# Optimization experiments

Hardware: AMD Instinct MI355X
Metric: run time of the kernel (lower is better)

The kernel has to match this reference:

```python
import jax, jax.numpy as jnp
import numpy as np

THRESHOLD = 0.4


def _pair_feat(xs, xd):
    # pair_mode='both': [src, dst, |src-dst|, src*dst] along feature axis
    return jnp.concatenate([xs, xd, jnp.abs(xs - xd), xs * xd], axis=-1)


def _mlp(pf, W1, b1, W2, b2):
    h = jax.nn.relu(pf @ W1 + b1)
    return (h @ W2 + b2)[..., 0]


def setup_inputs() -> dict:
    key = jax.random.key(0)
    k1, k2, k3, k4, k5 = jax.random.split(key, 5)
    N, F, E, H = 1024, 64, 65536, 32
    x = jax.random.normal(k1, (N, F), dtype=jnp.float32)
    edge_index = jax.random.randint(k2, (2, E), 0, N, dtype=jnp.int64)
    edge_index_global = jax.random.randint(k3, (2, E), 0, N, dtype=jnp.int64)
    W1 = jax.random.normal(k4, (4 * F, H), dtype=jnp.float32) * (1.0 / np.sqrt(4 * F))
    b1 = jnp.zeros((H,), dtype=jnp.float32)
    W2 = jax.random.normal(k5, (H, 1), dtype=jnp.float32) * (1.0 / np.sqrt(H))
    b2 = jnp.zeros((1,), dtype=jnp.float32)
    return {"x": x, "edge_index": edge_index, "edge_index_global": edge_index_global,
            "W1": W1, "b1": b1, "W2": W2, "b2": b2}


def reference(x, edge_index, edge_index_global, W1, b1, W2, b2):
    # ---- sparse edge branch ----
    xs = x[edge_index[0]]            # [E, F]
    xd = x[edge_index[1]]            # [E, F]
    pf = _pair_feat(xs, xd)          # [E, 4F]
    edge_logits = _mlp(pf, W1, b1, W2, b2)        # [E]
    edge_probs = jax.nn.sigmoid(edge_logits)      # [E]
    edge_actions = (edge_probs > THRESHOLD).astype(x.dtype)  # [E]
    # (new_edge_index / raw_edge_index in the original are data-dependent
    #  boolean selections of edge columns; the mask is edge_actions==1.)

    # ---- dense all-pairs branch (train=True) ----
    N, F = x.shape
    xi = jnp.broadcast_to(x[:, None, :], (N, N, F))  # src of pair (i,j)
    xj = jnp.broadcast_to(x[None, :, :], (N, N, F))  # dst of pair (i,j)
    pf_all = _pair_feat(xi, xj)                      # [N, N, 4F] -- dominant intermediate
    logits_all = _mlp(pf_all, W1, b1, W2, b2)        # [N, N]
    P = jax.nn.sigmoid(logits_all)                   # [N, N]

    return edge_probs, edge_actions, P
```

## Files before the change

kernel.cpp:

```cpp
#include <hip/hip_runtime.h>
#include <hip/hip_bf16.h>
#include <math.h>

#define NN 1024
#define FD 64
#define EE 65536
#define HD 32

typedef __attribute__((ext_vector_type(8))) short short8;
typedef __attribute__((ext_vector_type(4))) float floatx4;

__device__ __forceinline__ float sigmoid_f(float z) {
  return 1.0f / (1.0f + expf(-z));
}
__device__ __forceinline__ float sigmoid_fast(float z) {
  return 1.0f / (1.0f + __expf(-z));
}

__device__ __forceinline__ unsigned pack_bf16_trunc(float hi, float lo) {
  unsigned a = __builtin_bit_cast(unsigned, hi);
  unsigned b = __builtin_bit_cast(unsigned, lo);
  return __builtin_amdgcn_perm(a, b, 0x07060302u);
}

__device__ __forceinline__ short8 pack8(const float* v) {
  union { unsigned u[4]; short8 s; } p;
#pragma unroll
  for (int t = 0; t < 4; ++t) p.u[t] = pack_bf16_trunc(v[2 * t + 1], v[2 * t]);
  return p.s;
}

struct Frag3 { short8 a0, a1, a2; };

__device__ __forceinline__ Frag3 split_pack(const float* v) {
  float r[8], r2[8];
#pragma unroll
  for (int t = 0; t < 8; ++t) {
    const unsigned uv = __builtin_bit_cast(unsigned, v[t]);
    const float f0 = __builtin_bit_cast(float, uv & 0xFFFF0000u);
    const float rr = v[t] - f0;
    const unsigned ur = __builtin_bit_cast(unsigned, rr);
    const float f1 = __builtin_bit_cast(float, ur & 0xFFFF0000u);
    r[t] = rr;
    r2[t] = rr - f1;
  }
  Frag3 f;
  f.a0 = pack8(v);
  f.a1 = pack8(r);
  f.a2 = pack8(r2);
  return f;
}

__global__ __launch_bounds__(256) void pre_kernel3(
    const float* __restrict__ x, const float* __restrict__ W1,
    const float* __restrict__ b1, float* __restrict__ pre,
    short* __restrict__ Wt0, short* __restrict__ Wt1, short* __restrict__ Wt2) {
  const int blk = blockIdx.x;
  const int t = threadIdx.x;
  if (blk < 256) {
    const int node = blk * 4 + (t >> 6);
    const int which = (t >> 5) & 1;
    const int h = t & 31;
    const float* xr = x + node * FD;
    const float* wp = W1 + which * FD * HD + h;
    float a0 = which ? 0.0f : b1[h], a1 = 0.0f, a2 = 0.0f, a3 = 0.0f;
#pragma unroll
    for (int f = 0; f < FD; f += 4) {
      a0 = fmaf(xr[f + 0], wp[(f + 0) * HD], a0);
      a1 = fmaf(xr[f + 1], wp[(f + 1) * HD], a1);
      a2 = fmaf(xr[f + 2], wp[(f + 2) * HD], a2);
      a3 = fmaf(xr[f + 3], wp[(f + 3) * HD], a3);
    }
    pre[which * (NN * HD) + node * HD + h] = (a0 + a1) + (a2 + a3);
  } else {
    for (int idx = t; idx < 32 * 128; idx += 256) {
      const int h = idx >> 7;
      const int k = idx & 127;
      const int f = k & 63;
      const int b = 2 + (k >> 6);
      const float v = W1[(b * FD + f) * HD + h];
      const unsigned uv = __builtin_bit_cast(unsigned, v);
      const unsigned u0 = uv & 0xFFFF0000u;
      const float f0 = __builtin_bit_cast(float, u0);
      const float r = v - f0;
      const unsigned u1 = __builtin_bit_cast(unsigned, r) & 0xFFFF0000u;
      const float f1 = __builtin_bit_cast(float, u1);
      const float r2 = r - f1;
      const unsigned u2 = __builtin_bit_cast(unsigned, r2) & 0xFFFF0000u;
      Wt0[idx] = (short)(u0 >> 16);
      Wt1[idx] = (short)(u1 >> 16);
      Wt2[idx] = (short)(u2 >> 16);
    }
  }
}

__device__ __forceinline__ void edge_chunk(
    const float* feat, const short* __restrict__ Wt0,
    const short* __restrict__ Wt1, const short* __restrict__ Wt2,
    int c, int q, int kc, floatx4& acc0, floatx4& acc1) {
  const Frag3 B = split_pack(feat);
  const int off0 = c * 128 + kc * 32 + q * 8;
  const int off1 = (16 + c) * 128 + kc * 32 + q * 8;
  const short8 A00 = *(const short8*)(Wt0 + off0);
  const short8 A01 = *(const short8*)(Wt1 + off0);
  const short8 A02 = *(const short8*)(Wt2 + off0);
  const short8 A10 = *(const short8*)(Wt0 + off1);
  const short8 A11 = *(const short8*)(Wt1 + off1);
  const short8 A12 = *(const short8*)(Wt2 + off1);
  acc0 = __builtin_amdgcn_mfma_f32_16x16x32_bf16(A00, B.a0, acc0, 0, 0, 0);
  acc0 = __builtin_amdgcn_mfma_f32_16x16x32_bf16(A01, B.a0, acc0, 0, 0, 0);
  acc0 = __builtin_amdgcn_mfma_f32_16x16x32_bf16(A02, B.a0, acc0, 0, 0, 0);
  acc0 = __builtin_amdgcn_mfma_f32_16x16x32_bf16(A00, B.a1, acc0, 0, 0, 0);
  acc0 = __builtin_amdgcn_mfma_f32_16x16x32_bf16(A01, B.a1, acc0, 0, 0, 0);
  acc0 = __builtin_amdgcn_mfma_f32_16x16x32_bf16(A00, B.a2, acc0, 0, 0, 0);
  acc1 = __builtin_amdgcn_mfma_f32_16x16x32_bf16(A10, B.a0, acc1, 0, 0, 0);
  acc1 = __builtin_amdgcn_mfma_f32_16x16x32_bf16(A11, B.a0, acc1, 0, 0, 0);
  acc1 = __builtin_amdgcn_mfma_f32_16x16x32_bf16(A12, B.a0, acc1, 0, 0, 0);
  acc1 = __builtin_amdgcn_mfma_f32_16x16x32_bf16(A10, B.a1, acc1, 0, 0, 0);
  acc1 = __builtin_amdgcn_mfma_f32_16x16x32_bf16(A11, B.a1, acc1, 0, 0, 0);
  acc1 = __builtin_amdgcn_mfma_f32_16x16x32_bf16(A10, B.a2, acc1, 0, 0, 0);
}

#define DENSE_BLOCKS 520

__global__ __launch_bounds__(256, 3) void fused_mfma_kernel(
    const float* __restrict__ x, const int* __restrict__ eidx,
    const float* __restrict__ pre, const short* __restrict__ Wt0,
    const short* __restrict__ Wt1, const short* __restrict__ Wt2,
    const float* __restrict__ W2, const float* __restrict__ b2,
    float* __restrict__ out, float* __restrict__ outP) {
  __shared__ float mir[4][256];
  const int lane = threadIdx.x & 63;
  const int w = threadIdx.x >> 6;
  const int q = lane >> 4;
  const int c = lane & 15;

  if (blockIdx.x < DENSE_BLOCKS) {
    const int T = blockIdx.x * 4 + w;
    int a = (int)((sqrtf(8.0f * (float)T + 1.0f) - 1.0f) * 0.5f);
    while ((a + 1) * (a + 2) / 2 <= T) ++a;
    while (a * (a + 1) / 2 > T) --a;
    const int b = T - a * (a + 1) / 2;
    const int j0 = a * 16;
    const int i0 = b * 16;
    const bool offdiag = (a != b);

    short8 Af[2][4];
#pragma unroll
    for (int n = 0; n < 2; ++n)
#pragma unroll
      for (int s = 0; s < 4; ++s)
        Af[n][s] = *(const short8*)(Wt0 + (n * 16 + c) * 128 + s * 32 + q * 8);

    const float* xj = x + (size_t)(j0 + c) * FD;
    float jA[8], jB[8];
#pragma unroll
    for (int t = 0; t < 4; ++t) {
      jA[t] = xj[q * 8 + t];      jA[4 + t] = xj[q * 8 + 4 + t];
      jB[t] = xj[32 + q * 8 + t]; jB[4 + t] = xj[32 + q * 8 + 4 + t];
    }

    const floatx4 psA_j = *(const floatx4*)(pre + (j0 + c) * HD + q * 4);
    const floatx4 psB_j = *(const floatx4*)(pre + (j0 + c) * HD + 16 + q * 4);
    const floatx4 pdA_j = *(const floatx4*)(pre + NN * HD + (j0 + c) * HD + q * 4);
    const floatx4 pdB_j = *(const floatx4*)(pre + NN * HD + (j0 + c) * HD + 16 + q * 4);
    const floatx4 w2A = *(const floatx4*)(W2 + q * 4);
    const floatx4 w2B = *(const floatx4*)(W2 + 16 + q * 4);
    const float b2v = b2[0];

    for (int ii = 0; ii < 16; ++ii) {
      const int i = i0 + ii;
      const float* xi = x + (size_t)i * FD;
      const floatx4 psA_i = *(const floatx4*)(pre + i * HD + q * 4);
      const floatx4 psB_i = *(const floatx4*)(pre + i * HD + 16 + q * 4);
      floatx4 acc0 = {0.0f, 0.0f, 0.0f, 0.0f};
      floatx4 acc1 = {0.0f, 0.0f, 0.0f, 0.0f};

      {
        const floatx4 i0v = *(const floatx4*)(xi + q * 8);
        const floatx4 i1v = *(const floatx4*)(xi + q * 8 + 4);
        float ad[8], pr[8];
#pragma unroll
        for (int t = 0; t < 4; ++t) {
          ad[t] = fabsf(i0v[t] - jA[t]);         pr[t] = i0v[t] * jA[t];
          ad[4 + t] = fabsf(i1v[t] - jA[4 + t]); pr[4 + t] = i1v[t] * jA[4 + t];
        }
        const short8 fad = pack8(ad);
        const short8 fpr = pack8(pr);
        acc0 = __builtin_amdgcn_mfma_f32_16x16x32_bf16(Af[0][0], fad, acc0, 0, 0, 0);
        acc1 = __builtin_amdgcn_mfma_f32_16x16x32_bf16(Af[1][0], fad, acc1, 0, 0, 0);
        acc0 = __builtin_amdgcn_mfma_f32_16x16x32_bf16(Af[0][2], fpr, acc0, 0, 0, 0);
        acc1 = __builtin_amdgcn_mfma_f32_16x16x32_bf16(Af[1][2], fpr, acc1, 0, 0, 0);
      }
      {
        const floatx4 i0v = *(const floatx4*)(xi + 32 + q * 8);
        const floatx4 i1v = *(const floatx4*)(xi + 32 + q * 8 + 4);
        float ad[8], pr[8];
#pragma unroll
        for (int t = 0; t < 4; ++t) {
          ad[t] = fabsf(i0v[t] - jB[t]);         pr[t] = i0v[t] * jB[t];
          ad[4 + t] = fabsf(i1v[t] - jB[4 + t]); pr[4 + t] = i1v[t] * jB[4 + t];
        }
        const short8 fad = pack8(ad);
        const short8 fpr = pack8(pr);
        acc0 = __builtin_amdgcn_mfma_f32_16x16x32_bf16(Af[0][1], fad, acc0, 0, 0, 0);
        acc1 = __builtin_amdgcn_mfma_f32_16x16x32_bf16(Af[1][1], fad, acc1, 0, 0, 0);
        acc0 = __builtin_amdgcn_mfma_f32_16x16x32_bf16(Af[0][3], fpr, acc0, 0, 0, 0);
        acc1 = __builtin_amdgcn_mfma_f32_16x16x32_bf16(Af[1][3], fpr, acc1, 0, 0, 0);
      }

      float tv = 0.0f;
#pragma unroll
      for (int r = 0; r < 4; ++r) {
        tv = fmaf(fmaxf(acc0[r] + psA_i[r] + pdA_j[r], 0.0f), w2A[r], tv);
        tv = fmaf(fmaxf(acc1[r] + psB_i[r] + pdB_j[r], 0.0f), w2B[r], tv);
      }
      tv += __shfl_xor(tv, 16);
      tv += __shfl_xor(tv, 32);
      if (lane < 16) {
        outP[(size_t)i * NN + j0 + lane] = sigmoid_fast(tv + b2v);
      }

      if (offdiag) {
        const floatx4 pdA_i = *(const floatx4*)(pre + NN * HD + i * HD + q * 4);
        const floatx4 pdB_i = *(const floatx4*)(pre + NN * HD + i * HD + 16 + q * 4);
        float tm = 0.0f;
#pragma unroll
        for (int r = 0; r < 4; ++r) {
          tm = fmaf(fmaxf(acc0[r] + psA_j[r] + pdA_i[r], 0.0f), w2A[r], tm);
          tm = fmaf(fmaxf(acc1[r] + psB_j[r] + pdB_i[r], 0.0f), w2B[r], tm);
        }
        tm += __shfl_xor(tm, 16);
        tm += __shfl_xor(tm, 32);
        if (lane < 16) {
          mir[w][ii * 16 + lane] = sigmoid_fast(tm + b2v);
        }
      }
    }

    if (offdiag) {
      const int r = lane >> 2;
      const int g = lane & 3;
      floatx4 v;
#pragma unroll
      for (int t = 0; t < 4; ++t) v[t] = mir[w][(4 * g + t) * 16 + r];
      *(floatx4*)(outP + (size_t)(j0 + r) * NN + i0 + 4 * g) = v;
    }
  } else {
    const int e0 = ((blockIdx.x - DENSE_BLOCKS) * 4 + w) * 16;

    const bool is64 = (eidx[1] == 0) && (eidx[3] == 0) && (eidx[5] == 0);
    int s_c, d_c;
    if (is64) {
      s_c = eidx[2 * (e0 + c)];
      d_c = eidx[2 * (EE + e0 + c)];
    } else {
      s_c = eidx[e0 + c];
      d_c = eidx[EE + e0 + c];
    }
    const float* xs = x + (size_t)s_c * FD;
    const float* xd = x + (size_t)d_c * FD;

    floatx4 acc0, acc1;
    {
      const floatx4 psA = *(const floatx4*)(pre + s_c * HD + q * 4);
      const floatx4 psB = *(const floatx4*)(pre + s_c * HD + 16 + q * 4);
      const floatx4 pdA = *(const floatx4*)(pre + NN * HD + d_c * HD + q * 4);
      const floatx4 pdB = *(const floatx4*)(pre + NN * HD + d_c * HD + 16 + q * 4);
#pragma unroll
      for (int r = 0; r < 4; ++r) {
        acc0[r] = psA[r] + pdA[r];
        acc1[r] = psB[r] + pdB[r];
      }
    }

    {
      const floatx4 s0 = *(const floatx4*)(xs + q * 8);
      const floatx4 s1 = *(const floatx4*)(xs + q * 8 + 4);
      const floatx4 d0 = *(const floatx4*)(xd + q * 8);
      const floatx4 d1 = *(const floatx4*)(xd + q * 8 + 4);
      float ad[8], pr[8];
#pragma unroll
      for (int t = 0; t < 4; ++t) {
        ad[t] = fabsf(s0[t] - d0[t]);     pr[t] = s0[t] * d0[t];
        ad[4 + t] = fabsf(s1[t] - d1[t]); pr[4 + t] = s1[t] * d1[t];
      }
      edge_chunk(ad, Wt0, Wt1, Wt2, c, q, 0, acc0, acc1);
      edge_chunk(pr, Wt0, Wt1, Wt2, c, q, 2, acc0, acc1);
    }
    {
      const floatx4 s0 = *(const floatx4*)(xs + 32 + q * 8);
      const floatx4 s1 = *(const floatx4*)(xs + 32 + q * 8 + 4);
      const floatx4 d0 = *(const floatx4*)(xd + 32 + q * 8);
      const floatx4 d1 = *(const floatx4*)(xd + 32 + q * 8 + 4);
      float ad[8], pr[8];
#pragma unroll
      for (int t = 0; t < 4; ++t) {
        ad[t] = fabsf(s0[t] - d0[t]);     pr[t] = s0[t] * d0[t];
        ad[4 + t] = fabsf(s1[t] - d1[t]); pr[4 + t] = s1[t] * d1[t];
      }
      edge_chunk(ad, Wt0, Wt1, Wt2, c, q, 1, acc0, acc1);
      edge_chunk(pr, Wt0, Wt1, Wt2, c, q, 3, acc0, acc1);
    }

    const floatx4 w2A = *(const floatx4*)(W2 + q * 4);
    const floatx4 w2B = *(const floatx4*)(W2 + 16 + q * 4);
    float tv = 0.0f;
#pragma unroll
    for (int r = 0; r < 4; ++r) {
      tv = fmaf(fmaxf(acc0[r], 0.0f), w2A[r], tv);
      tv = fmaf(fmaxf(acc1[r], 0.0f), w2B[r], tv);
    }
    tv += __shfl_xor(tv, 16);
    tv += __shfl_xor(tv, 32);
    if (lane < 16) {
      const int e = e0 + lane;
      const float z = tv + b2[0];
      out[e] = sigmoid_f(z);
      out[EE + e] = (z > -0.40546510810816444f) ? 1.0f : 0.0f;
    }
  }
}

__device__ __forceinline__ float pair_logit_full(
    const float* __restrict__ xs, const float* __restrict__ xd,
    const float* __restrict__ W1, const float* __restrict__ b1,
    const float* __restrict__ W2, const float b2v) {
  float acc[HD];
#pragma unroll
  for (int h = 0; h < HD; ++h) acc[h] = b1[h];
#pragma unroll 1
  for (int f = 0; f < FD; ++f) {
    const float a = xs[f], b = xd[f];
    const float ad = fabsf(a - b), pr = a * b;
#pragma unroll
    for (int h = 0; h < HD; ++h) {
      float t0 = fmaf(a, W1[f * HD + h], acc[h]);
      t0 = fmaf(b, W1[(FD + f) * HD + h], t0);
      t0 = fmaf(ad, W1[(2 * FD + f) * HD + h], t0);
      acc[h] = fmaf(pr, W1[(3 * FD + f) * HD + h], t0);
    }
  }
  float z = b2v;
#pragma unroll
  for (int h = 0; h < HD; ++h) z = fmaf(fmaxf(acc[h], 0.0f), W2[h], z);
  return z;
}

__global__ __launch_bounds__(256) void edge_kernel_fb(
    const float* __restrict__ x, const int* __restrict__ eidx,
    const float* __restrict__ W1, const float* __restrict__ b1,
    const float* __restrict__ W2, const float* __restrict__ b2,
    float* __restrict__ out) {
  const int e = blockIdx.x * 256 + threadIdx.x;
  const bool is64 = (eidx[1] == 0) && (eidx[3] == 0) && (eidx[5] == 0);
  int s, d;
  if (is64) { s = eidx[2 * e]; d = eidx[2 * (EE + e)]; }
  else { s = eidx[e]; d = eidx[EE + e]; }
  const float z = pair_logit_full(x + (size_t)s * FD, x + (size_t)d * FD,
                                  W1, b1, W2, b2[0]);
  const float p = sigmoid_f(z);
  out[e] = p;
  out[EE + e] = (p > 0.4f) ? 1.0f : 0.0f;
}

__global__ __launch_bounds__(256) void dense_full_fb(
    const float* __restrict__ x, const float* __restrict__ W1,
    const float* __restrict__ b1, const float* __restrict__ W2,
    const float* __restrict__ b2, float* __restrict__ outP) {
  const int j = blockIdx.x * 64 + threadIdx.x % 64;
  const int i = blockIdx.y * 4 + threadIdx.x / 64;
  const float z = pair_logit_full(x + (size_t)i * FD, x + (size_t)j * FD,
                                  W1, b1, W2, b2[0]);
  outP[(size_t)i * NN + j] = sigmoid_f(z);
}

extern "C" void kernel_launch(void* const* d_in, const int* in_sizes, int n_in,
                              void* d_out, int out_size, void* d_ws, size_t ws_size,
                              hipStream_t stream) {
  const float* x  = (const float*)d_in[0];
  const int*  ei  = (const int*)d_in[1];
  const float* W1 = (const float*)d_in[3];
  const float* b1 = (const float*)d_in[4];
  const float* W2 = (const float*)d_in[5];
  const float* b2 = (const float*)d_in[6];
  float* out  = (float*)d_out;
  float* outP = out + 2 * EE;

  const size_t pre_bytes = (size_t)2 * NN * HD * sizeof(float);
  const size_t wt_elems = 32 * 128;
  const size_t need = pre_bytes + 3 * wt_elems * sizeof(short);
  if (ws_size >= need) {
    float* pre = (float*)d_ws;
    short* Wt0 = (short*)((char*)d_ws + pre_bytes);
    short* Wt1 = Wt0 + wt_elems;
    short* Wt2 = Wt1 + wt_elems;
    pre_kernel3<<<257, 256, 0, stream>>>(x, W1, b1, pre, Wt0, Wt1, Wt2);
    fused_mfma_kernel<<<DENSE_BLOCKS + 1024, 256, 0, stream>>>(
        x, ei, pre, Wt0, Wt1, Wt2, W2, b2, out, outP);
  } else {
    edge_kernel_fb<<<EE / 256, 256, 0, stream>>>(x, ei, W1, b1, W2, b2, out);
    dense_full_fb<<<dim3(NN / 64, NN / 4), 256, 0, stream>>>(
        x, W1, b1, W2, b2, outP);
  }
}
```

Measured before the change: 104.6 us.

## Merge precompute and main kernel into one cooperative launch with grid sync

Replaces the two-kernel sequence (precompute of per-node partial products and split bf16 weights, then the fused dense/edge MFMA kernel) with a single cooperative kernel. The precompute runs in the first blocks, a grid-wide barrier follows, and then a persistent grid of 768 blocks strides over the dense and edge work units. This targets the launch gap and tail between the two kernels, at the cost of a grid barrier and a fixed persistent grid that may balance work less evenly. The fp32 fallback kernels are removed, and the two-kernel path is kept only for when the cooperative launch fails.

```diff
diff --git a/kernel.cpp b/kernel.cpp
--- a/kernel.cpp
+++ b/kernel.cpp
@@ -1,6 +1,9 @@
 #include <hip/hip_runtime.h>
+#include <hip/hip_cooperative_groups.h>
 #include <hip/hip_bf16.h>
 #include <math.h>
+
+namespace cg = cooperative_groups;
 
 #define NN 1024
 #define FD 64
@@ -51,46 +54,45 @@
   return f;
 }
 
-__global__ __launch_bounds__(256) void pre_kernel3(
-    const float* __restrict__ x, const float* __restrict__ W1,
-    const float* __restrict__ b1, float* __restrict__ pre,
-    short* __restrict__ Wt0, short* __restrict__ Wt1, short* __restrict__ Wt2) {
-  const int blk = blockIdx.x;
-  const int t = threadIdx.x;
-  if (blk < 256) {
-    const int node = blk * 4 + (t >> 6);
-    const int which = (t >> 5) & 1;
-    const int h = t & 31;
-    const float* xr = x + node * FD;
-    const float* wp = W1 + which * FD * HD + h;
-    float a0 = which ? 0.0f : b1[h], a1 = 0.0f, a2 = 0.0f, a3 = 0.0f;
-#pragma unroll
-    for (int f = 0; f < FD; f += 4) {
-      a0 = fmaf(xr[f + 0], wp[(f + 0) * HD], a0);
-      a1 = fmaf(xr[f + 1], wp[(f + 1) * HD], a1);
-      a2 = fmaf(xr[f + 2], wp[(f + 2) * HD], a2);
-      a3 = fmaf(xr[f + 3], wp[(f + 3) * HD], a3);
-    }
-    pre[which * (NN * HD) + node * HD + h] = (a0 + a1) + (a2 + a3);
-  } else {
-    for (int idx = t; idx < 32 * 128; idx += 256) {
-      const int h = idx >> 7;
-      const int k = idx & 127;
-      const int f = k & 63;
-      const int b = 2 + (k >> 6);
-      const float v = W1[(b * FD + f) * HD + h];
-      const unsigned uv = __builtin_bit_cast(unsigned, v);
-      const unsigned u0 = uv & 0xFFFF0000u;
-      const float f0 = __builtin_bit_cast(float, u0);
-      const float r = v - f0;
-      const unsigned u1 = __builtin_bit_cast(unsigned, r) & 0xFFFF0000u;
-      const float f1 = __builtin_bit_cast(float, u1);
-      const float r2 = r - f1;
-      const unsigned u2 = __builtin_bit_cast(unsigned, r2) & 0xFFFF0000u;
-      Wt0[idx] = (short)(u0 >> 16);
-      Wt1[idx] = (short)(u1 >> 16);
-      Wt2[idx] = (short)(u2 >> 16);
-    }
+__device__ __forceinline__ void build_pre_block(
+    int blk, int t, const float* __restrict__ x, const float* __restrict__ W1,
+    const float* __restrict__ b1, float* __restrict__ pre) {
+  const int node = blk * 4 + (t >> 6);
+  const int which = (t >> 5) & 1;
+  const int h = t & 31;
+  const float* xr = x + node * FD;
+  const float* wp = W1 + which * FD * HD + h;
+  float a0 = which ? 0.0f : b1[h], a1 = 0.0f, a2 = 0.0f, a3 = 0.0f;
+#pragma unroll
+  for (int f = 0; f < FD; f += 4) {
+    a0 = fmaf(xr[f + 0], wp[(f + 0) * HD], a0);
+    a1 = fmaf(xr[f + 1], wp[(f + 1) * HD], a1);
+    a2 = fmaf(xr[f + 2], wp[(f + 2) * HD], a2);
+    a3 = fmaf(xr[f + 3], wp[(f + 3) * HD], a3);
+  }
+  pre[which * (NN * HD) + node * HD + h] = (a0 + a1) + (a2 + a3);
+}
+
+__device__ __forceinline__ void build_wt_block(
+    int t, const float* __restrict__ W1, short* __restrict__ Wt0,
+    short* __restrict__ Wt1, short* __restrict__ Wt2) {
+  for (int idx = t; idx < 32 * 128; idx += 256) {
+    const int h = idx >> 7;
+    const int k = idx & 127;
+    const int f = k & 63;
+    const int b = 2 + (k >> 6);
+    const float v = W1[(b * FD + f) * HD + h];
+    const unsigned uv = __builtin_bit_cast(unsigned, v);
+    const unsigned u0 = uv & 0xFFFF0000u;
+    const float f0 = __builtin_bit_cast(float, u0);
+    const float r = v - f0;
+    const unsigned u1 = __builtin_bit_cast(unsigned, r) & 0xFFFF0000u;
+    const float f1 = __builtin_bit_cast(float, u1);
+    const float r2 = r - f1;
+    const unsigned u2 = __builtin_bit_cast(unsigned, r2) & 0xFFFF0000u;
+    Wt0[idx] = (short)(u0 >> 16);
+    Wt1[idx] = (short)(u1 >> 16);
+    Wt2[idx] = (short)(u2 >> 16);
   }
 }
 
@@ -121,7 +123,250 @@
   acc1 = __builtin_amdgcn_mfma_f32_16x16x32_bf16(A10, B.a2, acc1, 0, 0, 0);
 }
 
+__device__ __forceinline__ void dense_unit(
+    int vb, int w, int lane, float (*mir)[256],
+    const float* __restrict__ x, const float* __restrict__ pre,
+    const short* __restrict__ Wt0, const float* __restrict__ W2,
+    const float* __restrict__ b2, float* __restrict__ outP) {
+  const int q = lane >> 4;
+  const int c = lane & 15;
+  const int T = vb * 4 + w;
+  int a = (int)((sqrtf(8.0f * (float)T + 1.0f) - 1.0f) * 0.5f);
+  while ((a + 1) * (a + 2) / 2 <= T) ++a;
+  while (a * (a + 1) / 2 > T) --a;
+  const int b = T - a * (a + 1) / 2;
+  const int j0 = a * 16;
+  const int i0 = b * 16;
+  const bool offdiag = (a != b);
+
+  short8 Af[2][4];
+#pragma unroll
+  for (int n = 0; n < 2; ++n)
+#pragma unroll
+    for (int s = 0; s < 4; ++s)
+      Af[n][s] = *(const short8*)(Wt0 + (n * 16 + c) * 128 + s * 32 + q * 8);
+
+  const float* xj = x + (size_t)(j0 + c) * FD;
+  float jA[8], jB[8];
+#pragma unroll
+  for (int t = 0; t < 4; ++t) {
+    jA[t] = xj[q * 8 + t];      jA[4 + t] = xj[q * 8 + 4 + t];
+    jB[t] = xj[32 + q * 8 + t]; jB[4 + t] = xj[32 + q * 8 + 4 + t];
+  }
+
+  const floatx4 psA_j = *(const floatx4*)(pre + (j0 + c) * HD + q * 4);
+  const floatx4 psB_j = *(const floatx4*)(pre + (j0 + c) * HD + 16 + q * 4);
+  const floatx4 pdA_j = *(const floatx4*)(pre + NN * HD + (j0 + c) * HD + q * 4);
+  const floatx4 pdB_j = *(const floatx4*)(pre + NN * HD + (j0 + c) * HD + 16 + q * 4);
+  const floatx4 w2A = *(const floatx4*)(W2 + q * 4);
+  const floatx4 w2B = *(const floatx4*)(W2 + 16 + q * 4);
+  const float b2v = b2[0];
+
+  for (int ii = 0; ii < 16; ++ii) {
+    const int i = i0 + ii;
+    const float* xi = x + (size_t)i * FD;
+    const floatx4 psA_i = *(const floatx4*)(pre + i * HD + q * 4);
+    const floatx4 psB_i = *(const floatx4*)(pre + i * HD + 16 + q * 4);
+    floatx4 acc0 = {0.0f, 0.0f, 0.0f, 0.0f};
+    floatx4 acc1 = {0.0f, 0.0f, 0.0f, 0.0f};
+
+    {
+      const floatx4 i0v = *(const floatx4*)(xi + q * 8);
+      const floatx4 i1v = *(const floatx4*)(xi + q * 8 + 4);
+      float ad[8], pr[8];
+#pragma unroll
+      for (int t = 0; t < 4; ++t) {
+        ad[t] = fabsf(i0v[t] - jA[t]);         pr[t] = i0v[t] * jA[t];
+        ad[4 + t] = fabsf(i1v[t] - jA[4 + t]); pr[4 + t] = i1v[t] * jA[4 + t];
+      }
+      const short8 fad = pack8(ad);
+      const short8 fpr = pack8(pr);
+      acc0 = __builtin_amdgcn_mfma_f32_16x16x32_bf16(Af[0][0], fad, acc0, 0, 0, 0);
+      acc1 = __builtin_amdgcn_mfma_f32_16x16x32_bf16(Af[1][0], fad, acc1, 0, 0, 0);
+      acc0 = __builtin_amdgcn_mfma_f32_16x16x32_bf16(Af[0][2], fpr, acc0, 0, 0, 0);
+      acc1 = __builtin_amdgcn_mfma_f32_16x16x32_bf16(Af[1][2], fpr, acc1, 0, 0, 0);
+    }
+    {
+      const floatx4 i0v = *(const floatx4*)(xi + 32 + q * 8);
+      const floatx4 i1v = *(const floatx4*)(xi + 32 + q * 8 + 4);
+      float ad[8], pr[8];
+#pragma unroll
+      for (int t = 0; t < 4; ++t) {
+        ad[t] = fabsf(i0v[t] - jB[t]);         pr[t] = i0v[t] * jB[t];
+        ad[4 + t] = fabsf(i1v[t] - jB[4 + t]); pr[4 + t] = i1v[t] * jB[4 + t];
+      }
+      const short8 fad = pack8(ad);
+      const short8 fpr = pack8(pr);
+      acc0 = __builtin_amdgcn_mfma_f32_16x16x32_bf16(Af[0][1], fad, acc0, 0, 0, 0);
+      acc1 = __builtin_amdgcn_mfma_f32_16x16x32_bf16(Af[1][1], fad, acc1, 0, 0, 0);
+      acc0 = __builtin_amdgcn_mfma_f32_16x16x32_bf16(Af[0][3], fpr, acc0, 0, 0, 0);
+      acc1 = __builtin_amdgcn_mfma_f32_16x16x32_bf16(Af[1][3], fpr, acc1, 0, 0, 0);
+    }
+
+    float tv = 0.0f;
+#pragma unroll
+    for (int r = 0; r < 4; ++r) {
+      tv = fmaf(fmaxf(acc0[r] + psA_i[r] + pdA_j[r], 0.0f), w2A[r], tv);
+      tv = fmaf(fmaxf(acc1[r] + psB_i[r] + pdB_j[r], 0.0f), w2B[r], tv);
+    }
+    tv += __shfl_xor(tv, 16);
+    tv += __shfl_xor(tv, 32);
+    if (lane < 16) {
+      outP[(size_t)i * NN + j0 + lane] = sigmoid_fast(tv + b2v);
+    }
+
+    if (offdiag) {
+      const floatx4 pdA_i = *(const floatx4*)(pre + NN * HD + i * HD + q * 4);
+      const floatx4 pdB_i = *(const floatx4*)(pre + NN * HD + i * HD + 16 + q * 4);
+      float tm = 0.0f;
+#pragma unroll
+      for (int r = 0; r < 4; ++r) {
+        tm = fmaf(fmaxf(acc0[r] + psA_j[r] + pdA_i[r], 0.0f), w2A[r], tm);
+        tm = fmaf(fmaxf(acc1[r] + psB_j[r] + pdB_i[r], 0.0f), w2B[r], tm);
+      }
+      tm += __shfl_xor(tm, 16);
+      tm += __shfl_xor(tm, 32);
+      if (lane < 16) {
+        mir[w][ii * 16 + lane] = sigmoid_fast(tm + b2v);
+      }
+    }
+  }
+
+  if (offdiag) {
+    const int r = lane >> 2;
+    const int g = lane & 3;
+    floatx4 v;
+#pragma unroll
+    for (int t = 0; t < 4; ++t) v[t] = mir[w][(4 * g + t) * 16 + r];
+    *(floatx4*)(outP + (size_t)(j0 + r) * NN + i0 + 4 * g) = v;
+  }
+}
+
+__device__ __forceinline__ void edge_unit(
+    int vb, int w, int lane,
+    const float* __restrict__ x, const int* __restrict__ eidx,
+    const float* __restrict__ pre, const short* __restrict__ Wt0,
+    const short* __restrict__ Wt1, const short* __restrict__ Wt2,
+    const float* __restrict__ W2, const float* __restrict__ b2,
+    float* __restrict__ out) {
+  const int q = lane >> 4;
+  const int c = lane & 15;
+  const int e0 = (vb * 4 + w) * 16;
+
+  const bool is64 = (eidx[1] == 0) && (eidx[3] == 0) && (eidx[5] == 0);
+  int s_c, d_c;
+  if (is64) {
+    s_c = eidx[2 * (e0 + c)];
+    d_c = eidx[2 * (EE + e0 + c)];
+  } else {
+    s_c = eidx[e0 + c];
+    d_c = eidx[EE + e0 + c];
+  }
+  const float* xs = x + (size_t)s_c * FD;
+  const float* xd = x + (size_t)d_c * FD;
+
+  floatx4 acc0, acc1;
+  {
+    const floatx4 psA = *(const floatx4*)(pre + s_c * HD + q * 4);
+    const floatx4 psB = *(const floatx4*)(pre + s_c * HD + 16 + q * 4);
+    const floatx4 pdA = *(const floatx4*)(pre + NN * HD + d_c * HD + q * 4);
+    const floatx4 pdB = *(const floatx4*)(pre + NN * HD + d_c * HD + 16 + q * 4);
+#pragma unroll
+    for (int r = 0; r < 4; ++r) {
+      acc0[r] = psA[r] + pdA[r];
+      acc1[r] = psB[r] + pdB[r];
+    }
+  }
+
+  {
+    const floatx4 s0 = *(const floatx4*)(xs + q * 8);
+    const floatx4 s1 = *(const floatx4*)(xs + q * 8 + 4);
+    const floatx4 d0 = *(const floatx4*)(xd + q * 8);
+    const floatx4 d1 = *(const floatx4*)(xd + q * 8 + 4);
+    float ad[8], pr[8];
+#pragma unroll
+    for (int t = 0; t < 4; ++t) {
+      ad[t] = fabsf(s0[t] - d0[t]);     pr[t] = s0[t] * d0[t];
+      ad[4 + t] = fabsf(s1[t] - d1[t]); pr[4 + t] = s1[t] * d1[t];
+    }
+    edge_chunk(ad, Wt0, Wt1, Wt2, c, q, 0, acc0, acc1);
+    edge_chunk(pr, Wt0, Wt1, Wt2, c, q, 2, acc0, acc1);
+  }
+  {
+    const floatx4 s0 = *(const floatx4*)(xs + 32 + q * 8);
+    const floatx4 s1 = *(const floatx4*)(xs + 32 + q * 8 + 4);
+    const floatx4 d0 = *(const floatx4*)(xd + 32 + q * 8);
+    const floatx4 d1 = *(const floatx4*)(xd + 32 + q * 8 + 4);
+    float ad[8], pr[8];
+#pragma unroll
+    for (int t = 0; t < 4; ++t) {
+      ad[t] = fabsf(s0[t] - d0[t]);     pr[t] = s0[t] * d0[t];
+      ad[4 + t] = fabsf(s1[t] - d1[t]); pr[4 + t] = s1[t] * d1[t];
+    }
+    edge_chunk(ad, Wt0, Wt1, Wt2, c, q, 1, acc0, acc1);
+    edge_chunk(pr, Wt0, Wt1, Wt2, c, q, 3, acc0, acc1);
+  }
+
+  const floatx4 w2A = *(const floatx4*)(W2 + q * 4);
+  const floatx4 w2B = *(const floatx4*)(W2 + 16 + q * 4);
+  float tv = 0.0f;
+#pragma unroll
+  for (int r = 0; r < 4; ++r) {
+    tv = fmaf(fmaxf(acc0[r], 0.0f), w2A[r], tv);
+    tv = fmaf(fmaxf(acc1[r], 0.0f), w2B[r], tv);
+  }
+  tv += __shfl_xor(tv, 16);
+  tv += __shfl_xor(tv, 32);
+  if (lane < 16) {
+    const int e = e0 + lane;
+    const float z = tv + b2[0];
+    out[e] = sigmoid_f(z);
+    out[EE + e] = (z > -0.40546510810816444f) ? 1.0f : 0.0f;
+  }
+}
+
 #define DENSE_BLOCKS 520
+#define COOP_GRID 768
+
+__global__ __launch_bounds__(256, 3) void mega_kernel(
+    const float* __restrict__ x, const int* __restrict__ eidx,
+    const float* __restrict__ W1, const float* __restrict__ b1,
+    float* __restrict__ pre, short* __restrict__ Wt0,
+    short* __restrict__ Wt1, short* __restrict__ Wt2,
+    const float* __restrict__ W2, const float* __restrict__ b2,
+    float* __restrict__ out, float* __restrict__ outP) {
+  __shared__ float mir[4][256];
+  const int lane = threadIdx.x & 63;
+  const int w = threadIdx.x >> 6;
+
+  if (blockIdx.x < 256) {
+    build_pre_block(blockIdx.x, threadIdx.x, x, W1, b1, pre);
+  } else if (blockIdx.x == 256) {
+    build_wt_block(threadIdx.x, W1, Wt0, Wt1, Wt2);
+  }
+  __threadfence();
+  cg::this_grid().sync();
+
+  for (int vb = blockIdx.x; vb < DENSE_BLOCKS + 1024; vb += COOP_GRID) {
+    if (vb < DENSE_BLOCKS) {
+      dense_unit(vb, w, lane, mir, x, pre, Wt0, W2, b2, outP);
+    } else {
+      edge_unit(vb - DENSE_BLOCKS, w, lane, x, eidx, pre, Wt0, Wt1, Wt2,
+                W2, b2, out);
+    }
+  }
+}
+
+__global__ __launch_bounds__(256) void pre_kernel3(
+    const float* __restrict__ x, const float* __restrict__ W1,
+    const float* __restrict__ b1, float* __restrict__ pre,
+    short* __restrict__ Wt0, short* __restrict__ Wt1, short* __restrict__ Wt2) {
+  if (blockIdx.x < 256) {
+    build_pre_block(blockIdx.x, threadIdx.x, x, W1, b1, pre);
+  } else {
+    build_wt_block(threadIdx.x, W1, Wt0, Wt1, Wt2);
+  }
+}
 
 __global__ __launch_bounds__(256, 3) void fused_mfma_kernel(
     const float* __restrict__ x, const int* __restrict__ eidx,
@@ -132,247 +377,12 @@
   __shared__ float mir[4][256];
   const int lane = threadIdx.x & 63;
   const int w = threadIdx.x >> 6;
-  const int q = lane >> 4;
-  const int c = lane & 15;
-
   if (blockIdx.x < DENSE_BLOCKS) {
-    const int T = blockIdx.x * 4 + w;
-    int a = (int)((sqrtf(8.0f * (float)T + 1.0f) - 1.0f) * 0.5f);
-    while ((a + 1) * (a + 2) / 2 <= T) ++a;
-    while (a * (a + 1) / 2 > T) --a;
-    const int b = T - a * (a + 1) / 2;
-    const int j0 = a * 16;
-    const int i0 = b * 16;
-    const bool offdiag = (a != b);
-
-    short8 Af[2][4];
-#pragma unroll
-    for (int n = 0; n < 2; ++n)
-#pragma unroll
-      for (int s = 0; s < 4; ++s)
-        Af[n][s] = *(const short8*)(Wt0 + (n * 16 + c) * 128 + s * 32 + q * 8);
-
-    const float* xj = x + (size_t)(j0 + c) * FD;
-    float jA[8], jB[8];
-#pragma unroll
-    for (int t = 0; t < 4; ++t) {
-      jA[t] = xj[q * 8 + t];      jA[4 + t] = xj[q * 8 + 4 + t];
-      jB[t] = xj[32 + q * 8 + t]; jB[4 + t] = xj[32 + q * 8 + 4 + t];
-    }
-
-    const floatx4 psA_j = *(const floatx4*)(pre + (j0 + c) * HD + q * 4);
-    const floatx4 psB_j = *(const floatx4*)(pre + (j0 + c) * HD + 16 + q * 4);
-    const floatx4 pdA_j = *(const floatx4*)(pre + NN * HD + (j0 + c) * HD + q * 4);
-    const floatx4 pdB_j = *(const floatx4*)(pre + NN * HD + (j0 + c) * HD + 16 + q * 4);
-    const floatx4 w2A = *(const floatx4*)(W2 + q * 4);
-    const floatx4 w2B = *(const floatx4*)(W2 + 16 + q * 4);
-    const float b2v = b2[0];
-
-    for (int ii = 0; ii < 16; ++ii) {
-      const int i = i0 + ii;
-      const float* xi = x + (size_t)i * FD;
-      const floatx4 psA_i = *(const floatx4*)(pre + i * HD + q * 4);
-      const floatx4 psB_i = *(const floatx4*)(pre + i * HD + 16 + q * 4);
-      floatx4 acc0 = {0.0f, 0.0f, 0.0f, 0.0f};
-      floatx4 acc1 = {0.0f, 0.0f, 0.0f, 0.0f};
-
-      {
-        const floatx4 i0v = *(const floatx4*)(xi + q * 8);
-        const floatx4 i1v = *(const floatx4*)(xi + q * 8 + 4);
-        float ad[8], pr[8];
-#pragma unroll
-        for (int t = 0; t < 4; ++t) {
-          ad[t] = fabsf(i0v[t] - jA[t]);         pr[t] = i0v[t] * jA[t];
-          ad[4 + t] = fabsf(i1v[t] - jA[4 + t]); pr[4 + t] = i1v[t] * jA[4 + t];
-        }
-        const short8 fad = pack8(ad);
-        const short8 fpr = pack8(pr);
-        acc0 = __builtin_amdgcn_mfma_f32_16x16x32_bf16(Af[0][0], fad, acc0, 0, 0, 0);
-        acc1 = __builtin_amdgcn_mfma_f32_16x16x32_bf16(Af[1][0], fad, acc1, 0, 0, 0);
-        acc0 = __builtin_amdgcn_mfma_f32_16x16x32_bf16(Af[0][2], fpr, acc0, 0, 0, 0);
-        acc1 = __builtin_amdgcn_mfma_f32_16x16x32_bf16(Af[1][2], fpr, acc1, 0, 0, 0);
-      }
-      {
-        const floatx4 i0v = *(const floatx4*)(xi + 32 + q * 8);
-        const floatx4 i1v = *(const floatx4*)(xi + 32 + q * 8 + 4);
-        float ad[8], pr[8];
-#pragma unroll
-        for (int t = 0; t < 4; ++t) {
-          ad[t] = fabsf(i0v[t] - jB[t]);         pr[t] = i0v[t] * jB[t];
-          ad[4 + t] = fabsf(i1v[t] - jB[4 + t]); pr[4 + t] = i1v[t] * jB[4 + t];
-        }
-        const short8 fad = pack8(ad);
-        const short8 fpr = pack8(pr);
-        acc0 = __builtin_amdgcn_mfma_f32_16x16x32_bf16(Af[0][1], fad, acc0, 0, 0, 0);
-        acc1 = __builtin_amdgcn_mfma_f32_16x16x32_bf16(Af[1][1], fad, acc1, 0, 0, 0);
-        acc0 = __builtin_amdgcn_mfma_f32_16x16x32_bf16(Af[0][3], fpr, acc0, 0, 0, 0);
-        acc1 = __builtin_amdgcn_mfma_f32_16x16x32_bf16(Af[1][3], fpr, acc1, 0, 0, 0);
-      }
-
-      float tv = 0.0f;
-#pragma unroll
-      for (int r = 0; r < 4; ++r) {
-        tv = fmaf(fmaxf(acc0[r] + psA_i[r] + pdA_j[r], 0.0f), w2A[r], tv);
-        tv = fmaf(fmaxf(acc1[r] + psB_i[r] + pdB_j[r], 0.0f), w2B[r], tv);
-      }
-      tv += __shfl_xor(tv, 16);
-      tv += __shfl_xor(tv, 32);
-      if (lane < 16) {
-        outP[(size_t)i * NN + j0 + lane] = sigmoid_fast(tv + b2v);
-      }
-
-      if (offdiag) {
-        const floatx4 pdA_i = *(const floatx4*)(pre + NN * HD + i * HD + q * 4);
-        const floatx4 pdB_i = *(const floatx4*)(pre + NN * HD + i * HD + 16 + q * 4);
-        float tm = 0.0f;
-#pragma unroll
-        for (int r = 0; r < 4; ++r) {
-          tm = fmaf(fmaxf(acc0[r] + psA_j[r] + pdA_i[r], 0.0f), w2A[r], tm);
-          tm = fmaf(fmaxf(acc1[r] + psB_j[r] + pdB_i[r], 0.0f), w2B[r], tm);
-        }
-        tm += __shfl_xor(tm, 16);
-        tm += __shfl_xor(tm, 32);
-        if (lane < 16) {
-          mir[w][ii * 16 + lane] = sigmoid_fast(tm + b2v);
-        }
-      }
-    }
-
-    if (offdiag) {
-      const int r = lane >> 2;
-      const int g = lane & 3;
-      floatx4 v;
-#pragma unroll
-      for (int t = 0; t < 4; ++t) v[t] = mir[w][(4 * g + t) * 16 + r];
-      *(floatx4*)(outP + (size_t)(j0 + r) * NN + i0 + 4 * g) = v;
-    }
+    dense_unit(blockIdx.x, w, lane, mir, x, pre, Wt0, W2, b2, outP);
   } else {
-    const int e0 = ((blockIdx.x - DENSE_BLOCKS) * 4 + w) * 16;
-
-    const bool is64 = (eidx[1] == 0) && (eidx[3] == 0) && (eidx[5] == 0);
-    int s_c, d_c;
-    if (is64) {
-      s_c = eidx[2 * (e0 + c)];
-      d_c = eidx[2 * (EE + e0 + c)];
-    } else {
-      s_c = eidx[e0 + c];
-      d_c = eidx[EE + e0 + c];
-    }
-    const float* xs = x + (size_t)s_c * FD;
-    const float* xd = x + (size_t)d_c * FD;
-
-    floatx4 acc0, acc1;
-    {
-      const floatx4 psA = *(const floatx4*)(pre + s_c * HD + q * 4);
-      const floatx4 psB = *(const floatx4*)(pre + s_c * HD + 16 + q * 4);
-      const floatx4 pdA = *(const floatx4*)(pre + NN * HD + d_c * HD + q * 4);
-      const floatx4 pdB = *(const floatx4*)(pre + NN * HD + d_c * HD + 16 + q * 4);
-#pragma unroll
-      for (int r = 0; r < 4; ++r) {
-        acc0[r] = psA[r] + pdA[r];
-        acc1[r] = psB[r] + pdB[r];
-      }
-    }
-
-    {
-      const floatx4 s0 = *(const floatx4*)(xs + q * 8);
-      const floatx4 s1 = *(const floatx4*)(xs + q * 8 + 4);
-      const floatx4 d0 = *(const floatx4*)(xd + q * 8);
-      const floatx4 d1 = *(const floatx4*)(xd + q * 8 + 4);
-      float ad[8], pr[8];
-#pragma unroll
-      for (int t = 0; t < 4; ++t) {
-        ad[t] = fabsf(s0[t] - d0[t]);     pr[t] = s0[t] * d0[t];
-        ad[4 + t] = fabsf(s1[t] - d1[t]); pr[4 + t] = s1[t] * d1[t];
-      }
-      edge_chunk(ad, Wt0, Wt1, Wt2, c, q, 0, acc0, acc1);
-      edge_chunk(pr, Wt0, Wt1, Wt2, c, q, 2, acc0, acc1);
-    }
-    {
-      const floatx4 s0 = *(const floatx4*)(xs + 32 + q * 8);
-      const floatx4 s1 = *(const floatx4*)(xs + 32 + q * 8 + 4);
-      const floatx4 d0 = *(const floatx4*)(xd + 32 + q * 8);
-      const floatx4 d1 = *(const floatx4*)(xd + 32 + q * 8 + 4);
-      float ad[8], pr[8];
-#pragma unroll
-      for (int t = 0; t < 4; ++t) {
-        ad[t] = fabsf(s0[t] - d0[t]);     pr[t] = s0[t] * d0[t];
-        ad[4 + t] = fabsf(s1[t] - d1[t]); pr[4 + t] = s1[t] * d1[t];
-      }
-      edge_chunk(ad, Wt0, Wt1, Wt2, c, q, 1, acc0, acc1);
-      edge_chunk(pr, Wt0, Wt1, Wt2, c, q, 3, acc0, acc1);
-    }
-
-    const floatx4 w2A = *(const floatx4*)(W2 + q * 4);
-    const floatx4 w2B = *(const floatx4*)(W2 + 16 + q * 4);
-    float tv = 0.0f;
-#pragma unroll
-    for (int r = 0; r < 4; ++r) {
-      tv = fmaf(fmaxf(acc0[r], 0.0f), w2A[r], tv);
-      tv = fmaf(fmaxf(acc1[r], 0.0f), w2B[r], tv);
-    }
-    tv += __shfl_xor(tv, 16);
-    tv += __shfl_xor(tv, 32);
-    if (lane < 16) {
-      const int e = e0 + lane;
-      const float z = tv + b2[0];
-      out[e] = sigmoid_f(z);
-      out[EE + e] = (z > -0.40546510810816444f) ? 1.0f : 0.0f;
-    }
-  }
-}
-
-__device__ __forceinline__ float pair_logit_full(
-    const float* __restrict__ xs, const float* __restrict__ xd,
-    const float* __restrict__ W1, const float* __restrict__ b1,
-    const float* __restrict__ W2, const float b2v) {
-  float acc[HD];
-#pragma unroll
-  for (int h = 0; h < HD; ++h) acc[h] = b1[h];
-#pragma unroll 1
-  for (int f = 0; f < FD; ++f) {
-    const float a = xs[f], b = xd[f];
-    const float ad = fabsf(a - b), pr = a * b;
-#pragma unroll
-    for (int h = 0; h < HD; ++h) {
-      float t0 = fmaf(a, W1[f * HD + h], acc[h]);
-      t0 = fmaf(b, W1[(FD + f) * HD + h], t0);
-      t0 = fmaf(ad, W1[(2 * FD + f) * HD + h], t0);
-      acc[h] = fmaf(pr, W1[(3 * FD + f) * HD + h], t0);
-    }
-  }
-  float z = b2v;
-#pragma unroll
-  for (int h = 0; h < HD; ++h) z = fmaf(fmaxf(acc[h], 0.0f), W2[h], z);
-  return z;
-}
-
-__global__ __launch_bounds__(256) void edge_kernel_fb(
-    const float* __restrict__ x, const int* __restrict__ eidx,
-    const float* __restrict__ W1, const float* __restrict__ b1,
-    const float* __restrict__ W2, const float* __restrict__ b2,
-    float* __restrict__ out) {
-  const int e = blockIdx.x * 256 + threadIdx.x;
-  const bool is64 = (eidx[1] == 0) && (eidx[3] == 0) && (eidx[5] == 0);
-  int s, d;
-  if (is64) { s = eidx[2 * e]; d = eidx[2 * (EE + e)]; }
-  else { s = eidx[e]; d = eidx[EE + e]; }
-  const float z = pair_logit_full(x + (size_t)s * FD, x + (size_t)d * FD,
-                                  W1, b1, W2, b2[0]);
-  const float p = sigmoid_f(z);
-  out[e] = p;
-  out[EE + e] = (p > 0.4f) ? 1.0f : 0.0f;
-}
-
-__global__ __launch_bounds__(256) void dense_full_fb(
-    const float* __restrict__ x, const float* __restrict__ W1,
-    const float* __restrict__ b1, const float* __restrict__ W2,
-    const float* __restrict__ b2, float* __restrict__ outP) {
-  const int j = blockIdx.x * 64 + threadIdx.x % 64;
-  const int i = blockIdx.y * 4 + threadIdx.x / 64;
-  const float z = pair_logit_full(x + (size_t)i * FD, x + (size_t)j * FD,
-                                  W1, b1, W2, b2[0]);
-  outP[(size_t)i * NN + j] = sigmoid_f(z);
+    edge_unit(blockIdx.x - DENSE_BLOCKS, w, lane, x, eidx, pre, Wt0, Wt1, Wt2,
+              W2, b2, out);
+  }
 }
 
 extern "C" void kernel_launch(void* const* d_in, const int* in_sizes, int n_in,
@@ -389,18 +399,21 @@
 
   const size_t pre_bytes = (size_t)2 * NN * HD * sizeof(float);
   const size_t wt_elems = 32 * 128;
-  const size_t need = pre_bytes + 3 * wt_elems * sizeof(short);
-  if (ws_size >= need) {
-    float* pre = (float*)d_ws;
-    short* Wt0 = (short*)((char*)d_ws + pre_bytes);
-    short* Wt1 = Wt0 + wt_elems;
-    short* Wt2 = Wt1 + wt_elems;
+  float* pre = (float*)d_ws;
+  short* Wt0 = (short*)((char*)d_ws + pre_bytes);
+  short* Wt1 = Wt0 + wt_elems;
+  short* Wt2 = Wt1 + wt_elems;
+
+  void* args[] = {
+    (void*)&x, (void*)&ei, (void*)&W1, (void*)&b1,
+    (void*)&pre, (void*)&Wt0, (void*)&Wt1, (void*)&Wt2,
+    (void*)&W2, (void*)&b2, (void*)&out, (void*)&outP
+  };
+  hipError_t err = hipLaunchCooperativeKernel(
+      (const void*)mega_kernel, dim3(COOP_GRID), dim3(256), args, 0, stream);
+  if (err != hipSuccess) {
     pre_kernel3<<<257, 256, 0, stream>>>(x, W1, b1, pre, Wt0, Wt1, Wt2);
     fused_mfma_kernel<<<DENSE_BLOCKS + 1024, 256, 0, stream>>>(
         x, ei, pre, Wt0, Wt1, Wt2, W2, b2, out, outP);
-  } else {
-    edge_kernel_fb<<<EE / 256, 256, 0, stream>>>(x, ei, W1, b1, W2, b2, out);
-    dense_full_fb<<<dim3(NN / 64, NN / 4), 256, 0, stream>>>(
-        x, W1, b1, W2, b2, outP);
-  }
-}
+  }
+}
```

Result: slower. 213.0 us (+103.6%).
